# Kernel optimization log

Measured on AMD Instinct MI355X. Metric: run time of the kernel, lower is better.

Reference implementation:

```python
import jax, jax.numpy as jnp
import numpy as np

FREQ_DIM = 32
TIME_DIM = 32
HEADS = 8
TWO_PI = 6.283185307179586


def get_embeddings(B, H, W, freq_dim, time_dim, dtype):
    # freq embeddings over the height (frequency) axis
    nf = freq_dim // 2
    ln_x = jnp.log2(jnp.arange(0, H * nf, dtype=jnp.float32))
    ln_x = ln_x.at[0].set(-2.0)
    ln_x = ln_x.reshape(H, nf).T  # [nf, H]
    ln_x = ln_x * jnp.arange(1, nf + 1, dtype=jnp.float32)[:, None]
    # view_as_real(exp(1j*theta)) -> (cos, sin), interleaved per order along channel dim
    freq = jnp.stack([jnp.cos(ln_x), jnp.sin(ln_x)], axis=1).reshape(freq_dim, H)  # [freq_dim, H]
    freq = jnp.broadcast_to(freq[None, :, :, None], (B, freq_dim, H, W))

    # time embeddings over the width (time) axis
    nt = time_dim // 2
    k = jnp.arange(0, nt, dtype=jnp.float32) + 0.5  # [nt]
    x = jnp.arange(0, nt * W, dtype=jnp.float32).reshape(W, nt).T  # [nt, W]
    theta = k[:, None] * x / (W * nt) * TWO_PI  # [nt, W]
    time = jnp.stack([jnp.cos(theta), jnp.sin(theta)], axis=1).reshape(time_dim, W)  # [time_dim, W]
    time = jnp.broadcast_to(time[None, :, None, :], (B, time_dim, H, W))

    return jnp.concatenate([freq, time], axis=1).astype(dtype)  # [B, freq_dim+time_dim, H, W]


def setup_inputs() -> dict:
    key = jax.random.key(0)
    ks = jax.random.split(key, 6)
    B, C, H, W = 2, 512, 64, 32
    qkC = C + FREQ_DIM + TIME_DIM  # 576
    inner = HEADS * 64  # 512
    return {
        "hidden_states": jax.random.normal(ks[0], (B, C, H, W), dtype=jnp.float32),
        "Wq": jax.random.normal(ks[1], (qkC, inner), dtype=jnp.float32) * 0.02,
        "Wk": jax.random.normal(ks[2], (qkC, inner), dtype=jnp.float32) * 0.02,
        "Wv": jax.random.normal(ks[3], (C, inner), dtype=jnp.float32) * 0.02,
        "Wout": jax.random.normal(ks[4], (inner, C), dtype=jnp.float32) * 0.02,
        "bout": jnp.zeros((C,), dtype=jnp.float32),
    }


def reference(hidden_states, Wq, Wk, Wv, Wout, bout):
    B, C, H, W = hidden_states.shape
    emb = get_embeddings(B, H, W, FREQ_DIM, TIME_DIM, hidden_states.dtype)
    qk_hs = jnp.concatenate([hidden_states, emb], axis=1)  # [B, qkC, H, W]

    S = H * W
    qk_hs = qk_hs.reshape(B, -1, S).transpose(0, 2, 1)  # [B, S, qkC]
    v_hs = hidden_states.reshape(B, C, S).transpose(0, 2, 1)  # [B, S, C]

    q = qk_hs @ Wq  # [B, S, inner]
    k = qk_hs @ Wk
    v = v_hs @ Wv

    hd_qk = q.shape[-1] // HEADS
    hd_v = v.shape[-1] // HEADS
    q = q.reshape(B, S, HEADS, hd_qk).transpose(0, 2, 1, 3)  # [B, h, S, d]
    k = k.reshape(B, S, HEADS, hd_qk).transpose(0, 2, 1, 3)
    v = v.reshape(B, S, HEADS, hd_v).transpose(0, 2, 1, 3)

    scale = 1.0 / jnp.sqrt(jnp.asarray(hd_qk, dtype=q.dtype))
    scores = jnp.einsum('bhqd,bhkd->bhqk', q, k) * scale
    attn = jax.nn.softmax(scores, axis=-1)
    o = jnp.einsum('bhqk,bhkd->bhqd', attn, v)  # [B, h, S, d_v]

    o = o.transpose(0, 2, 1, 3).reshape(B, S, HEADS * hd_v)
    o = o @ Wout + bout  # [B, S, C]
    o = o.transpose(0, 2, 1).reshape(B, C, H, W)

    return o + hidden_states  # residual_connection=True, rescale_output_factor=1.0
```

## Files before the change

### kernel.cpp

```cpp
#include <hip/hip_runtime.h>
#include <math.h>

#define B_    2
#define C_    512
#define H_    64
#define W_    32
#define S_    2048
#define QKC_  576
#define INNER_ 512
#define NH_   8
#define HD_   64
#define TWO_PI_ 6.283185307179586f

typedef __attribute__((ext_vector_type(8))) short bfrag;
typedef __attribute__((ext_vector_type(4))) float ffrag;
typedef __attribute__((ext_vector_type(16))) float f16v;

typedef __attribute__((address_space(1))) const unsigned int as1_u32;
typedef __attribute__((address_space(3))) unsigned int as3_u32;

__device__ __forceinline__ ushort f2bf(float f) {
    unsigned u = __builtin_bit_cast(unsigned, f);
    unsigned r = (u + 0x7FFFu + ((u >> 16) & 1u)) >> 16;
    return (ushort)r;
}

__device__ __forceinline__ f16v zero16() {
    f16v z;
    #pragma unroll
    for (int i = 0; i < 16; i++) z[i] = 0.f;
    return z;
}

#define GLD(gp_, lp_) __builtin_amdgcn_global_load_lds((as1_u32*)(gp_), (as3_u32*)(lp_), 16, 0, 0)
#define EXPA(dst_, x_) asm("v_exp_f32 %0, %1" : "=v"(dst_) : "v"(x_))
#define SC_LOG2E 0.18033688011f

__global__ void k_trans_emb(const float* __restrict__ hid, ushort* __restrict__ X) {
    __shared__ float t[32][33];
    int b  = blockIdx.z;
    int s0 = blockIdx.x * 32, c0 = blockIdx.y * 32;
    int tx = threadIdx.x, ty = threadIdx.y;
    if (c0 < 512) {
        t[ty][tx] = hid[((size_t)b * C_ + (c0 + ty)) * S_ + s0 + tx];
        __syncthreads();
        X[((size_t)(b * S_ + s0 + ty)) * QKC_ + c0 + tx] = f2bf(t[tx][ty]);
    } else {
        int c = c0 - 512 + tx;
        int s = s0 + ty;
        int h = s >> 5, w = s & 31;
        float val;
        if (c < 32) {
            int f = c >> 1;
            int n = h * 16 + f;
            float lx = (n == 0) ? -2.0f : log2f((float)n);
            float arg = lx * (float)(f + 1);
            val = (c & 1) ? sinf(arg) : cosf(arg);
        } else {
            int tt = (c - 32) >> 1;
            float theta = ((float)tt + 0.5f) * (float)(w * 16 + tt) * (TWO_PI_ / 512.0f);
            val = (c & 1) ? sinf(theta) : cosf(theta);
        }
        X[(size_t)(b * S_ + s) * QKC_ + c0 + tx] = f2bf(val);
    }
}

__global__ void k_wtrans_all(const float* __restrict__ Wq, const float* __restrict__ Wk,
                             const float* __restrict__ Wv, const float* __restrict__ Wo,
                             ushort* __restrict__ Wqt, ushort* __restrict__ Wkt,
                             ushort* __restrict__ Wvt, ushort* __restrict__ Wot) {
    __shared__ float t[32][33];
    int z = blockIdx.z;
    const float* W; ushort* Wt; int K;
    if (z == 0)      { W = Wq; Wt = Wqt; K = QKC_; }
    else if (z == 1) { W = Wk; Wt = Wkt; K = QKC_; }
    else if (z == 2) { W = Wv; Wt = Wvt; K = C_; }
    else             { W = Wo; Wt = Wot; K = INNER_; }
    int k0 = blockIdx.x * 32, n0 = blockIdx.y * 32;
    if (k0 >= K) return;
    int tx = threadIdx.x, ty = threadIdx.y;
    t[ty][tx] = W[(size_t)(k0 + ty) * 512 + n0 + tx];
    __syncthreads();
    Wt[(size_t)(n0 + ty) * K + k0 + tx] = f2bf(t[tx][ty]);
}

#define GSTAGE(buf_, k0_) {                                                   \
    _Pragma("unroll")                                                         \
    for (int i_ = 0; i_ < 6; i_++)                                            \
        GLD(gp[i_] + (k0_), tl + (buf_) * 12288 + lo[i_]); }

__global__ __launch_bounds__(256, 3) void k_qkv(const ushort* __restrict__ X,
                                                const ushort* __restrict__ Wqt,
                                                const ushort* __restrict__ Wkt,
                                                const ushort* __restrict__ Wvt,
                                                ushort* __restrict__ Qb,
                                                ushort* __restrict__ Kpk,
                                                ushort* __restrict__ Vpk) {
    __shared__ ushort __attribute__((aligned(16))) tl[2 * 12288];

    int tid = threadIdx.x;
    int l = tid & 63, wv = tid >> 6;
    int wr = wv >> 1, wc = wv & 1;
    int bid = blockIdx.x;
    int lgc = (bid & 7) * 96 + (bid >> 3);
    int bx = lgc % 24, by = lgc / 24;
    int n0 = bx * 64, m0 = by * 128;
    int sel = n0 >> 9, n0l = n0 & 511;
    const ushort* Bt = (sel == 0) ? Wqt : (sel == 1) ? Wkt : Wvt;
    const int K = (sel < 2) ? QKC_ : C_;
    const int nst = K >> 6;
    int l15 = l & 15, lg = l >> 4;
    int swz = l15 & 7;

    const ushort* gp[6];
    unsigned lo[6];
    {
        int rsub = l >> 3;
        int clog = (l & 7) ^ rsub;
        #pragma unroll
        for (int i = 0; i < 6; i++) {
            int c = wv * 6 + i;
            lo[i] = c * 512;
            if (c < 16) gp[i] = X  + (size_t)(m0  + c * 8        + rsub) * QKC_ + clog * 8;
            else        gp[i] = Bt + (size_t)(n0l + (c - 16) * 8 + rsub) * K    + clog * 8;
        }
    }

    ffrag acc[4][2];
    #pragma unroll
    for (int i = 0; i < 4; i++)
        #pragma unroll
        for (int j = 0; j < 2; j++) acc[i][j] = (ffrag){0.f, 0.f, 0.f, 0.f};

    GSTAGE(0, 0);
    int cur = 0;
    for (int kt = 0; kt < nst; kt++) {
        __syncthreads();
        if (kt + 1 < nst) GSTAGE(cur ^ 1, (kt + 1) * 64);
        const ushort* As = tl + cur * 12288;
        const ushort* Bs = As + 8192;
        #pragma unroll
        for (int ks = 0; ks < 2; ks++) {
            int cl = ks * 4 + lg;
            int ch = (cl ^ swz) * 8;
            bfrag af[4], bf[2];
            #pragma unroll
            for (int mi = 0; mi < 4; mi++)
                af[mi] = *(const bfrag*)(As + (wr * 64 + mi * 16 + l15) * 64 + ch);
            #pragma unroll
            for (int nj = 0; nj < 2; nj++)
                bf[nj] = *(const bfrag*)(Bs + (wc * 32 + nj * 16 + l15) * 64 + ch);
            #pragma unroll
            for (int mi = 0; mi < 4; mi++)
                #pragma unroll
                for (int nj = 0; nj < 2; nj++)
                    acc[mi][nj] = __builtin_amdgcn_mfma_f32_16x16x32_bf16(af[mi], bf[nj], acc[mi][nj], 0, 0, 0);
        }
        cur ^= 1;
    }

    if (sel == 0) {
        #pragma unroll
        for (int mi = 0; mi < 4; mi++)
            #pragma unroll
            for (int nj = 0; nj < 2; nj++)
                #pragma unroll
                for (int r = 0; r < 4; r++) {
                    int row = m0 + wr * 64 + mi * 16 + lg * 4 + r;
                    int col = n0l + wc * 32 + nj * 16 + l15;
                    Qb[(size_t)row * INNER_ + col] = f2bf(acc[mi][nj][r]);
                }
    } else {
        ushort (*Ct)[136] = (ushort(*)[136])tl;
        __syncthreads();
        #pragma unroll
        for (int mi = 0; mi < 4; mi++)
            #pragma unroll
            for (int nj = 0; nj < 2; nj++)
                #pragma unroll
                for (int r = 0; r < 4; r++)
                    Ct[wc * 32 + nj * 16 + l15][wr * 64 + mi * 16 + lg * 4 + r] = f2bf(acc[mi][nj][r]);
        __syncthreads();
        int pair = (m0 >> 11) * 8 + (n0l >> 6);
        int kvb0 = (m0 & 2047) >> 5;
        if (sel == 1) {
            #pragma unroll
            for (int p = 0; p < 4; p++) {
                int cid = tid + p * 256;
                int sl = cid >> 7, kv = cid & 127;
                bfrag tmp;
                #pragma unroll
                for (int j = 0; j < 8; j++) tmp[j] = (short)Ct[sl * 8 + j][kv];
                ushort* dst = Kpk + ((size_t)((pair * 64 + kvb0 + (kv >> 5)) * 8 + sl)) * 256 + (kv & 31) * 8;
                *(uint4*)dst = __builtin_bit_cast(uint4, tmp);
            }
        } else {
            #pragma unroll
            for (int p = 0; p < 4; p++) {
                int cid = tid + p * 256;
                int d = cid >> 4, mc = cid & 15;
                uint4 v = *(uint4*)&Ct[d][mc * 8];
                ushort* dst = Vpk + ((size_t)((pair * 64 + kvb0 + (mc >> 2)) * 4 + (mc & 3))) * 512 + d * 8;
                *(uint4*)dst = v;
            }
        }
    }
}

__global__ __launch_bounds__(256, 2) void k_og(const ushort* __restrict__ Ob,
                                               const ushort* __restrict__ Wot,
                                               const float* __restrict__ bias,
                                               const float* __restrict__ hid,
                                               float* __restrict__ out) {
    __shared__ ushort __attribute__((aligned(16))) tl[2 * 12288];

    int tid = threadIdx.x;
    int l = tid & 63, wv = tid >> 6;
    int wr = wv >> 1, wc = wv & 1;
    int bid = blockIdx.x;
    int lgc = (bid & 7) * 32 + (bid >> 3);
    int bx = lgc & 7, by = lgc >> 3;
    int n0 = bx * 64, m0 = by * 128;
    int l15 = l & 15, lg = l >> 4;
    int swz = l15 & 7;

    const ushort* gp[6];
    unsigned lo[6];
    {
        int rsub = l >> 3;
        int clog = (l & 7) ^ rsub;
        #pragma unroll
        for (int i = 0; i < 6; i++) {
            int c = wv * 6 + i;
            lo[i] = c * 512;
            if (c < 16) gp[i] = Ob  + (size_t)(m0 + c * 8        + rsub) * INNER_ + clog * 8;
            else        gp[i] = Wot + (size_t)(n0 + (c - 16) * 8 + rsub) * INNER_ + clog * 8;
        }
    }

    ffrag acc[4][2];
    #pragma unroll
    for (int i = 0; i < 4; i++)
        #pragma unroll
        for (int j = 0; j < 2; j++) acc[i][j] = (ffrag){0.f, 0.f, 0.f, 0.f};

    GSTAGE(0, 0);
    int cur = 0;
    for (int kt = 0; kt < 8; kt++) {
        __syncthreads();
        if (kt < 7) GSTAGE(cur ^ 1, (kt + 1) * 64);
        const ushort* As = tl + cur * 12288;
        const ushort* Bs = As + 8192;
        #pragma unroll
        for (int ks = 0; ks < 2; ks++) {
            int cl = ks * 4 + lg;
            int ch = (cl ^ swz) * 8;
            bfrag af[4], bf[2];
            #pragma unroll
            for (int mi = 0; mi < 4; mi++)
                af[mi] = *(const bfrag*)(As + (wr * 64 + mi * 16 + l15) * 64 + ch);
            #pragma unroll
            for (int nj = 0; nj < 2; nj++)
                bf[nj] = *(const bfrag*)(Bs + (wc * 32 + nj * 16 + l15) * 64 + ch);
            #pragma unroll
            for (int mi = 0; mi < 4; mi++)
                #pragma unroll
                for (int nj = 0; nj < 2; nj++)
                    acc[mi][nj] = __builtin_amdgcn_mfma_f32_16x16x32_bf16(af[mi], bf[nj], acc[mi][nj], 0, 0, 0);
        }
        cur ^= 1;
    }

    float (*Cf)[129] = (float(*)[129])tl;
    float bv[2];
    #pragma unroll
    for (int nj = 0; nj < 2; nj++) bv[nj] = bias[n0 + wc * 32 + nj * 16 + l15];
    __syncthreads();
    #pragma unroll
    for (int mi = 0; mi < 4; mi++)
        #pragma unroll
        for (int nj = 0; nj < 2; nj++)
            #pragma unroll
            for (int r = 0; r < 4; r++)
                Cf[wc * 32 + nj * 16 + l15][wr * 64 + mi * 16 + lg * 4 + r] = acc[mi][nj][r] + bv[nj];
    __syncthreads();
    int b = m0 >> 11, s0m = m0 & 2047;
    #pragma unroll
    for (int p = 0; p < 8; p++) {
        int f = p * 256 + tid;
        int c = f >> 5, sq = (f & 31) * 4;
        size_t o = (((size_t)(b * 512 + n0 + c)) << 11) + s0m + sq;
        float4 hv = *(const float4*)(hid + o);
        float4 cv = *(float4*)&Cf[c][sq];
        cv.x += hv.x; cv.y += hv.y; cv.z += hv.z; cv.w += hv.w;
        *(float4*)(out + o) = cv;
    }
}

#define CVTPK(dst, a, b) asm("v_cvt_pk_bf16_f32 %0, %1, %2" : "=v"(dst) : "v"(a), "v"(b))
#define SWAP32(a, b)     asm("v_permlane32_swap_b32 %0, %1" : "+v"(a), "+v"(b))

#define ASTAGE(buf_, kt_) {                                                   \
    const ushort* gk_ = kpb + (size_t)(kt_) * 2048 + l * 8;                   \
    const ushort* gv_ = vpb + (size_t)(kt_) * 2048 + l * 8;                   \
    ushort* lk_ = lbase + (buf_) * 4096;                                      \
    _Pragma("unroll")                                                         \
    for (int i_ = 0; i_ < 4; i_++) GLD(gk_ + i_ * 512, lk_ + i_ * 512);       \
    _Pragma("unroll")                                                         \
    for (int i_ = 0; i_ < 4; i_++) GLD(gv_ + i_ * 512, lk_ + 2048 + i_ * 512); }

#define AITER(bufc_, ktc_, a0_, a1_) {                                        \
    asm volatile("s_waitcnt lgkmcnt(0)" ::: "memory");                        \
    if ((ktc_) < 31) {                                                        \
        ASTAGE((bufc_) ^ 1, (ktc_) + 1);                                      \
        asm volatile("s_waitcnt vmcnt(8)" ::: "memory");                      \
    } else {                                                                  \
        asm volatile("s_waitcnt vmcnt(0)" ::: "memory");                      \
    }                                                                         \
    __builtin_amdgcn_sched_barrier(0);                                        \
    const ushort* Kt_ = lbase + (bufc_) * 4096;                               \
    const ushort* Vt_ = Kt_ + 2048;                                           \
    f16v sfA = zero16(), sfB = zero16();                                      \
    __builtin_amdgcn_s_setprio(1);                                            \
    sfA = __builtin_amdgcn_mfma_f32_32x32x16_bf16(*(const bfrag*)(Kt_ + 0 * 512 + koff), qf[0], sfA, 0, 0, 0); \
    sfB = __builtin_amdgcn_mfma_f32_32x32x16_bf16(*(const bfrag*)(Kt_ + 2 * 512 + koff), qf[2], sfB, 0, 0, 0); \
    sfA = __builtin_amdgcn_mfma_f32_32x32x16_bf16(*(const bfrag*)(Kt_ + 1 * 512 + koff), qf[1], sfA, 0, 0, 0); \
    sfB = __builtin_amdgcn_mfma_f32_32x32x16_bf16(*(const bfrag*)(Kt_ + 3 * 512 + koff), qf[3], sfB, 0, 0, 0); \
    __builtin_amdgcn_s_setprio(0);                                            \
    float ls0 = 0.f, ls1 = 0.f, ls2 = 0.f, ls3 = 0.f;                         \
    _Pragma("unroll")                                                         \
    for (int j = 0; j < 4; j++) {                                             \
        float pj0; EXPA(pj0, (sfA[j]      + sfB[j])      * SC_LOG2E);         \
        float pj1; EXPA(pj1, (sfA[j + 4]  + sfB[j + 4])  * SC_LOG2E);         \
        float pj2; EXPA(pj2, (sfA[j + 8]  + sfB[j + 8])  * SC_LOG2E);         \
        float pj3; EXPA(pj3, (sfA[j + 12] + sfB[j + 12]) * SC_LOG2E);         \
        sfA[j] = pj0; sfA[j + 4] = pj1; sfA[j + 8] = pj2; sfA[j + 12] = pj3;  \
        ls0 += pj0; ls1 += pj1; ls2 += pj2; ls3 += pj3;                       \
    }                                                                         \
    l_run += (ls0 + ls1) + (ls2 + ls3);                                       \
    __builtin_amdgcn_s_setprio(1);                                            \
    _Pragma("unroll")                                                         \
    for (int s = 0; s < 2; s++) {                                             \
        unsigned A0, B0, A1, B1;                                              \
        CVTPK(A0, sfA[s * 8 + 0], sfA[s * 8 + 1]); CVTPK(B0, sfA[s * 8 + 4], sfA[s * 8 + 5]); \
        SWAP32(A0, B0);                                                       \
        CVTPK(A1, sfA[s * 8 + 2], sfA[s * 8 + 3]); CVTPK(B1, sfA[s * 8 + 6], sfA[s * 8 + 7]); \
        SWAP32(A1, B1);                                                       \
        uint4 u_; u_.x = A0; u_.y = A1; u_.z = B0; u_.w = B1;                 \
        bfrag pa_ = __builtin_bit_cast(bfrag, u_);                            \
        bfrag v0_ = *(const bfrag*)(Vt_ + s * 1024 + voff);                   \
        bfrag v1_ = *(const bfrag*)(Vt_ + s * 1024 + voff + 256);             \
        a0_ = __builtin_amdgcn_mfma_f32_32x32x16_bf16(v0_, pa_, a0_, 0, 0, 0);\
        a1_ = __builtin_amdgcn_mfma_f32_32x32x16_bf16(v1_, pa_, a1_, 0, 0, 0);\
    }                                                                         \
    __builtin_amdgcn_s_setprio(0); }

__global__ __launch_bounds__(512, 2) void k_attn(const ushort* __restrict__ Qf,
                                                 const ushort* __restrict__ Kpk,
                                                 const ushort* __restrict__ Vpk,
                                                 ushort* __restrict__ Ob) {
    __shared__ __attribute__((aligned(16))) char smem[132096];
    ushort* ktv  = (ushort*)smem;
    float*  cmb  = (float*)smem;
    float*  lsh  = (float*)(smem + 131072);

    const int id  = blockIdx.x;
    const int xcd = id & 7, wi = id >> 3;
    const int pair = xcd * 2 + (wi >> 4);
    const int qt   = wi & 15;
    const int hd = pair & 7, b = pair >> 3;

    const int tid = threadIdx.x;
    const int l = tid & 63, wvid = tid >> 6;
    const int qi = wvid >> 1, sp = wvid & 1;
    const int l31 = l & 31, hi = l >> 5;
    const int hoff = hd * HD_;
    const int brow = b * S_ + qt * 128;

    bfrag qf[4];
    {
        const ushort* qp = Qf + (size_t)(brow + qi * 32 + l31) * INNER_ + hoff + hi * 8;
        #pragma unroll
        for (int ks = 0; ks < 4; ks++) qf[ks] = *(const bfrag*)(qp + ks * 16);
    }

    const ushort* kpb = Kpk + ((size_t)pair * 64 + sp * 32) * 2048;
    const ushort* vpb = Vpk + ((size_t)pair * 64 + sp * 32) * 2048;
    ushort* lbase = ktv + wvid * 8192;
    const int koff = l31 * 8 + hi * 256;
    const int voff = l31 * 8 + hi * 512;

    ASTAGE(0, 0);

    float l_run = 0.f;
    f16v acc0a = zero16(), acc1a = zero16();
    f16v acc0b = zero16(), acc1b = zero16();

    for (int it = 0; it < 16; it++) {
        AITER(0, it * 2,     acc0a, acc1a);
        AITER(1, it * 2 + 1, acc0b, acc1b);
    }

    f16v acc0 = acc0a, acc1 = acc1a;
    #pragma unroll
    for (int j = 0; j < 16; j++) { acc0[j] += acc0b[j]; acc1[j] += acc1b[j]; }
    l_run += __shfl_xor(l_run, 32);

    if (hi == 0) lsh[wvid * 32 + l31] = l_run;
    __syncthreads();
    {
        float* creg = cmb + wvid * 2112;
        #pragma unroll
        for (int j = 0; j < 16; j++) {
            int d0 = (j & 3) + 8 * (j >> 2) + 4 * hi;
            creg[d0 * 33 + l31]        = acc0[j];
            creg[(d0 + 32) * 33 + l31] = acc1[j];
        }
    }
    __syncthreads();
    #pragma unroll
    for (int p2 = 0; p2 < 2; p2++) {
        int f = p2 * 512 + tid;
        int qg4 = f >> 8;
        int t2 = f & 255;
        int qq = t2 >> 3, cc = t2 & 7;
        float lt = lsh[(qg4 * 2) * 32 + qq] + lsh[(qg4 * 2 + 1) * 32 + qq];
        float inv = 1.0f / lt;
        bfrag ov;
        #pragma unroll
        for (int j = 0; j < 8; j++) {
            int d = cc * 8 + j;
            float s = cmb[(qg4 * 2) * 2112 + d * 33 + qq] + cmb[(qg4 * 2 + 1) * 2112 + d * 33 + qq];
            ov[j] = (short)f2bf(s * inv);
        }
        *(uint4*)(Ob + (size_t)(brow + qg4 * 32 + qq) * INNER_ + hoff + cc * 8) = __builtin_bit_cast(uint4, ov);
    }
}

extern "C" void kernel_launch(void* const* d_in, const int* in_sizes, int n_in,
                              void* d_out, int out_size, void* d_ws, size_t ws_size,
                              hipStream_t stream) {
    const float* hid  = (const float*)d_in[0];
    const float* Wq   = (const float*)d_in[1];
    const float* Wk   = (const float*)d_in[2];
    const float* Wv   = (const float*)d_in[3];
    const float* Wout = (const float*)d_in[4];
    const float* bout = (const float*)d_in[5];
    float* out = (float*)d_out;

    const int M = B_ * S_;
    char* w = (char*)d_ws;
    ushort* X    = (ushort*)w;                    w += (size_t)M * QKC_ * 2;
    ushort* Qb   = (ushort*)w;                    w += (size_t)M * INNER_ * 2;
    ushort* Kpk  = (ushort*)w;                    w += (size_t)M * INNER_ * 2;
    ushort* Vpk  = (ushort*)w;                    w += (size_t)M * INNER_ * 2;
    ushort* Ob   = (ushort*)w;                    w += (size_t)M * INNER_ * 2;
    ushort* Wqt  = (ushort*)w;                    w += (size_t)INNER_ * QKC_ * 2;
    ushort* Wkt  = (ushort*)w;                    w += (size_t)INNER_ * QKC_ * 2;
    ushort* Wvt  = (ushort*)w;                    w += (size_t)INNER_ * C_ * 2;
    ushort* Wot  = (ushort*)w;                    w += (size_t)C_ * INNER_ * 2;

    k_wtrans_all<<<dim3(18, 16, 4), dim3(32, 32), 0, stream>>>(Wq, Wk, Wv, Wout,
                                                               Wqt, Wkt, Wvt, Wot);
    k_trans_emb<<<dim3(S_ / 32, 18, B_), dim3(32, 32), 0, stream>>>(hid, X);

    k_qkv<<<dim3(768), 256, 0, stream>>>(X, Wqt, Wkt, Wvt, Qb, Kpk, Vpk);

    k_attn<<<dim3(256), 512, 0, stream>>>(Qb, Kpk, Vpk, Ob);

    k_og<<<dim3(256), 256, 0, stream>>>(Ob, Wot, bout, hid, out);
}
```

Measured before the change: 66.26 us.

## Load K/V fragments directly into registers instead of staging through LDS

The attention kernel no longer copies K and V tiles into shared memory with global-to-LDS loads. It now reads MFMA fragments straight from global memory into double-buffered registers, prefetching the next tile while the current one is computed. This shrinks shared memory to about 68KB per block, so two 512-thread blocks can fit per CU, and it drops the LDS waits and one barrier. The cost is more register pressure and exposed global-load latency per wave. The score MFMAs also become a single serial accumulation chain rather than two independent ones.

```diff
diff --git a/kernel.cpp b/kernel.cpp
--- a/kernel.cpp
+++ b/kernel.cpp
@@ -300,58 +300,49 @@
 #define CVTPK(dst, a, b) asm("v_cvt_pk_bf16_f32 %0, %1, %2" : "=v"(dst) : "v"(a), "v"(b))
 #define SWAP32(a, b)     asm("v_permlane32_swap_b32 %0, %1" : "+v"(a), "+v"(b))
 
-#define ASTAGE(buf_, kt_) {                                                   \
-    const ushort* gk_ = kpb + (size_t)(kt_) * 2048 + l * 8;                   \
-    const ushort* gv_ = vpb + (size_t)(kt_) * 2048 + l * 8;                   \
-    ushort* lk_ = lbase + (buf_) * 4096;                                      \
+#define KLOAD(dst_, kt_) {                                                    \
+    const ushort* g_ = kpb + (size_t)(kt_) * 2048 + kro;                      \
     _Pragma("unroll")                                                         \
-    for (int i_ = 0; i_ < 4; i_++) GLD(gk_ + i_ * 512, lk_ + i_ * 512);       \
-    _Pragma("unroll")                                                         \
-    for (int i_ = 0; i_ < 4; i_++) GLD(gv_ + i_ * 512, lk_ + 2048 + i_ * 512); }
-
-#define AITER(bufc_, ktc_, a0_, a1_) {                                        \
-    asm volatile("s_waitcnt lgkmcnt(0)" ::: "memory");                        \
-    if ((ktc_) < 31) {                                                        \
-        ASTAGE((bufc_) ^ 1, (ktc_) + 1);                                      \
-        asm volatile("s_waitcnt vmcnt(8)" ::: "memory");                      \
-    } else {                                                                  \
-        asm volatile("s_waitcnt vmcnt(0)" ::: "memory");                      \
-    }                                                                         \
-    __builtin_amdgcn_sched_barrier(0);                                        \
-    const ushort* Kt_ = lbase + (bufc_) * 4096;                               \
-    const ushort* Vt_ = Kt_ + 2048;                                           \
-    f16v sfA = zero16(), sfB = zero16();                                      \
+    for (int ks_ = 0; ks_ < 4; ks_++) dst_[ks_] = *(const bfrag*)(g_ + ks_ * 512); }
+
+#define VLOAD(dst_, kt_) {                                                    \
+    const ushort* g_ = vpb + (size_t)(kt_) * 2048 + vro;                      \
+    dst_[0] = *(const bfrag*)(g_);                                            \
+    dst_[1] = *(const bfrag*)(g_ + 256);                                      \
+    dst_[2] = *(const bfrag*)(g_ + 1024);                                     \
+    dst_[3] = *(const bfrag*)(g_ + 1280); }
+
+#define ABODY(kf_, vf_, a0_, a1_) {                                           \
+    f16v sf = zero16();                                                       \
     __builtin_amdgcn_s_setprio(1);                                            \
-    sfA = __builtin_amdgcn_mfma_f32_32x32x16_bf16(*(const bfrag*)(Kt_ + 0 * 512 + koff), qf[0], sfA, 0, 0, 0); \
-    sfB = __builtin_amdgcn_mfma_f32_32x32x16_bf16(*(const bfrag*)(Kt_ + 2 * 512 + koff), qf[2], sfB, 0, 0, 0); \
-    sfA = __builtin_amdgcn_mfma_f32_32x32x16_bf16(*(const bfrag*)(Kt_ + 1 * 512 + koff), qf[1], sfA, 0, 0, 0); \
-    sfB = __builtin_amdgcn_mfma_f32_32x32x16_bf16(*(const bfrag*)(Kt_ + 3 * 512 + koff), qf[3], sfB, 0, 0, 0); \
+    sf = __builtin_amdgcn_mfma_f32_32x32x16_bf16(kf_[0], qf[0], sf, 0, 0, 0); \
+    sf = __builtin_amdgcn_mfma_f32_32x32x16_bf16(kf_[1], qf[1], sf, 0, 0, 0); \
+    sf = __builtin_amdgcn_mfma_f32_32x32x16_bf16(kf_[2], qf[2], sf, 0, 0, 0); \
+    sf = __builtin_amdgcn_mfma_f32_32x32x16_bf16(kf_[3], qf[3], sf, 0, 0, 0); \
     __builtin_amdgcn_s_setprio(0);                                            \
     float ls0 = 0.f, ls1 = 0.f, ls2 = 0.f, ls3 = 0.f;                         \
     _Pragma("unroll")                                                         \
     for (int j = 0; j < 4; j++) {                                             \
-        float pj0; EXPA(pj0, (sfA[j]      + sfB[j])      * SC_LOG2E);         \
-        float pj1; EXPA(pj1, (sfA[j + 4]  + sfB[j + 4])  * SC_LOG2E);         \
-        float pj2; EXPA(pj2, (sfA[j + 8]  + sfB[j + 8])  * SC_LOG2E);         \
-        float pj3; EXPA(pj3, (sfA[j + 12] + sfB[j + 12]) * SC_LOG2E);         \
-        sfA[j] = pj0; sfA[j + 4] = pj1; sfA[j + 8] = pj2; sfA[j + 12] = pj3;  \
-        ls0 += pj0; ls1 += pj1; ls2 += pj2; ls3 += pj3;                       \
+        float p0; EXPA(p0, sf[j]      * SC_LOG2E);                            \
+        float p1; EXPA(p1, sf[j + 4]  * SC_LOG2E);                            \
+        float p2; EXPA(p2, sf[j + 8]  * SC_LOG2E);                            \
+        float p3; EXPA(p3, sf[j + 12] * SC_LOG2E);                            \
+        sf[j] = p0; sf[j + 4] = p1; sf[j + 8] = p2; sf[j + 12] = p3;          \
+        ls0 += p0; ls1 += p1; ls2 += p2; ls3 += p3;                           \
     }                                                                         \
     l_run += (ls0 + ls1) + (ls2 + ls3);                                       \
     __builtin_amdgcn_s_setprio(1);                                            \
     _Pragma("unroll")                                                         \
     for (int s = 0; s < 2; s++) {                                             \
         unsigned A0, B0, A1, B1;                                              \
-        CVTPK(A0, sfA[s * 8 + 0], sfA[s * 8 + 1]); CVTPK(B0, sfA[s * 8 + 4], sfA[s * 8 + 5]); \
+        CVTPK(A0, sf[s * 8 + 0], sf[s * 8 + 1]); CVTPK(B0, sf[s * 8 + 4], sf[s * 8 + 5]); \
         SWAP32(A0, B0);                                                       \
-        CVTPK(A1, sfA[s * 8 + 2], sfA[s * 8 + 3]); CVTPK(B1, sfA[s * 8 + 6], sfA[s * 8 + 7]); \
+        CVTPK(A1, sf[s * 8 + 2], sf[s * 8 + 3]); CVTPK(B1, sf[s * 8 + 6], sf[s * 8 + 7]); \
         SWAP32(A1, B1);                                                       \
         uint4 u_; u_.x = A0; u_.y = A1; u_.z = B0; u_.w = B1;                 \
         bfrag pa_ = __builtin_bit_cast(bfrag, u_);                            \
-        bfrag v0_ = *(const bfrag*)(Vt_ + s * 1024 + voff);                   \
-        bfrag v1_ = *(const bfrag*)(Vt_ + s * 1024 + voff + 256);             \
-        a0_ = __builtin_amdgcn_mfma_f32_32x32x16_bf16(v0_, pa_, a0_, 0, 0, 0);\
-        a1_ = __builtin_amdgcn_mfma_f32_32x32x16_bf16(v1_, pa_, a1_, 0, 0, 0);\
+        a0_ = __builtin_amdgcn_mfma_f32_32x32x16_bf16(vf_[s * 2],     pa_, a0_, 0, 0, 0); \
+        a1_ = __builtin_amdgcn_mfma_f32_32x32x16_bf16(vf_[s * 2 + 1], pa_, a1_, 0, 0, 0); \
     }                                                                         \
     __builtin_amdgcn_s_setprio(0); }
 
@@ -359,10 +350,9 @@
                                                  const ushort* __restrict__ Kpk,
                                                  const ushort* __restrict__ Vpk,
                                                  ushort* __restrict__ Ob) {
-    __shared__ __attribute__((aligned(16))) char smem[132096];
-    ushort* ktv  = (ushort*)smem;
-    float*  cmb  = (float*)smem;
-    float*  lsh  = (float*)(smem + 131072);
+    __shared__ __attribute__((aligned(16))) char smem[68608];
+    float* cmb = (float*)smem;
+    float* lsh = (float*)(smem + 67584);
 
     const int id  = blockIdx.x;
     const int xcd = id & 7, wi = id >> 3;
@@ -386,19 +376,21 @@
 
     const ushort* kpb = Kpk + ((size_t)pair * 64 + sp * 32) * 2048;
     const ushort* vpb = Vpk + ((size_t)pair * 64 + sp * 32) * 2048;
-    ushort* lbase = ktv + wvid * 8192;
-    const int koff = l31 * 8 + hi * 256;
-    const int voff = l31 * 8 + hi * 512;
-
-    ASTAGE(0, 0);
+    const int kro = hi * 256 + l31 * 8;
+    const int vro = hi * 512 + l31 * 8;
 
     float l_run = 0.f;
     f16v acc0a = zero16(), acc1a = zero16();
     f16v acc0b = zero16(), acc1b = zero16();
 
-    for (int it = 0; it < 16; it++) {
-        AITER(0, it * 2,     acc0a, acc1a);
-        AITER(1, it * 2 + 1, acc0b, acc1b);
+    bfrag kc[4], vc[4], kn[4], vn[4];
+    KLOAD(kc, 0); VLOAD(vc, 0);
+
+    for (int it = 0; it < 32; it += 2) {
+        if (it + 1 < 32) { KLOAD(kn, it + 1); VLOAD(vn, it + 1); }
+        ABODY(kc, vc, acc0a, acc1a);
+        if (it + 2 < 32) { KLOAD(kc, it + 2); VLOAD(vc, it + 2); }
+        ABODY(kn, vn, acc0b, acc1b);
     }
 
     f16v acc0 = acc0a, acc1 = acc1a;
@@ -407,7 +399,6 @@
     l_run += __shfl_xor(l_run, 32);
 
     if (hi == 0) lsh[wvid * 32 + l31] = l_run;
-    __syncthreads();
     {
         float* creg = cmb + wvid * 2112;
         #pragma unroll
```

After: 60.81 us. -8.2%, faster.
